# Kernel optimization log

Hardware: AMD Instinct MI355X
Metric: run time of the kernel (lower is better)

## Reference

```python
import jax, jax.numpy as jnp
import numpy as np

N_HEAD = 12
ROPE_BASE = 10000.0


def rotate_half(x):
    h = x.shape[-1] // 2
    x1, x2 = x[..., :h], x[..., h:]
    return jnp.concatenate((-x2, x1), axis=-1)


def rope_cos_sin(T, head_dim, dtype):
    inv_freq = 1.0 / (ROPE_BASE ** (jnp.arange(0, head_dim, 2, dtype=jnp.float32) / head_dim))
    t = jnp.arange(T, dtype=jnp.float32)
    freqs = jnp.einsum('i,j->ij', t, inv_freq)          # [T, head_dim/2]
    emb = jnp.concatenate((freqs, freqs), axis=-1)       # [T, head_dim]
    return jnp.cos(emb).astype(dtype), jnp.sin(emb).astype(dtype)


def setup_inputs() -> dict:
    key = jax.random.key(0)
    ks = jax.random.split(key, 5)
    B, T, C = 1, 4096, 768
    return {
        'x': jax.random.normal(ks[0], (B, T, C), dtype=jnp.float32),
        'w_attn': jax.random.normal(ks[1], (C, 3 * C), dtype=jnp.float32) * (1.0 / np.sqrt(C)),
        'b_attn': jax.random.normal(ks[2], (3 * C,), dtype=jnp.float32) * 0.02,
        'w_proj': jax.random.normal(ks[3], (C, C), dtype=jnp.float32) * (1.0 / np.sqrt(C)),
        'b_proj': jax.random.normal(ks[4], (C,), dtype=jnp.float32) * 0.02,
    }


def reference(x, w_attn, b_attn, w_proj, b_proj):
    B, T, C = x.shape
    H = N_HEAD
    hd = C // H

    qkv = x @ w_attn + b_attn                            # [B, T, 3C]
    q, k, v = jnp.split(qkv, 3, axis=-1)
    q = q.reshape(B, T, H, hd)
    k = k.reshape(B, T, H, hd)
    v = v.reshape(B, T, H, hd)

    cos, sin = rope_cos_sin(T, hd, x.dtype)              # [T, hd]
    cos = cos[None, :, None, :]
    sin = sin[None, :, None, :]
    q = q * cos + rotate_half(q) * sin
    k = k * cos + rotate_half(k) * sin

    # [B, H, T, hd]
    q = q.transpose(0, 2, 1, 3)
    k = k.transpose(0, 2, 1, 3)
    v = v.transpose(0, 2, 1, 3)

    att = jnp.einsum('bhtd,bhsd->bhts', q, k) * (1.0 / np.sqrt(hd))
    causal_mask = jnp.triu(jnp.ones((T, T), dtype=bool), k=1)
    att = jnp.where(causal_mask, -jnp.inf, att)
    att = jax.nn.softmax(att, axis=-1)

    y = jnp.einsum('bhts,bhsd->bhtd', att, v)            # [B, H, T, hd]
    y = y.transpose(0, 2, 1, 3).reshape(B, T, C)
    return y @ w_proj + b_proj
```

## Files before the change

kernel.cpp:

```cpp
#include <hip/hip_runtime.h>
#include <hip/hip_bf16.h>
#include <math.h>

using bf16 = __hip_bfloat16;
typedef __bf16 bf16x8_t __attribute__((ext_vector_type(8)));
typedef float f32x4_t __attribute__((ext_vector_type(4)));

static __device__ __forceinline__ f32x4_t mfma16(bf16x8_t a, bf16x8_t b, f32x4_t c) {
    return __builtin_amdgcn_mfma_f32_16x16x32_bf16(a, b, c, 0, 0, 0);
}

#if __has_builtin(__builtin_amdgcn_exp2f)
#define EXP2F __builtin_amdgcn_exp2f
#else
#define EXP2F exp2f
#endif

static __device__ __forceinline__ void sincos_rev(float rev, float* s, float* c) {
    float f = rev - floorf(rev);
#if __has_builtin(__builtin_amdgcn_sinf) && __has_builtin(__builtin_amdgcn_cosf)
    *s = __builtin_amdgcn_sinf(f);
    *c = __builtin_amdgcn_cosf(f);
#else
    float th = f * 6.2831853071795864f;
    *s = __sinf(th); *c = __cosf(th);
#endif
}

static __device__ __forceinline__ void async16(bf16* lds, const bf16* g) {
#if __has_builtin(__builtin_amdgcn_global_load_lds)
    __builtin_amdgcn_global_load_lds(
        (const __attribute__((address_space(1))) unsigned int*)g,
        (__attribute__((address_space(3))) unsigned int*)lds, 16, 0, 0);
#else
    const int lane = threadIdx.x & 63;
    *reinterpret_cast<float4*>(lds + lane * 8) =
        *reinterpret_cast<const float4*>(g);
#endif
}

static __device__ __forceinline__ float bias_at(const void* b, int i, int isbf) {
    return isbf ? __bfloat162float(((const bf16*)b)[i]) : ((const float*)b)[i];
}

__global__ void detect_kernel(const unsigned short* __restrict__ u16, int* flag) {
    const int lane = threadIdx.x;
    int sane = 0;
#pragma unroll
    for (int j = 0; j < 4; ++j) {
        const unsigned short u = u16[2 * (lane * 4 + j)];
        const int e = (u >> 7) & 0xFF;
        if (u == 0 || (e >= 100 && e <= 150)) sane++;
    }
    for (int off = 32; off; off >>= 1) sane += __shfl_down(sane, off);
    if (lane == 0) *flag = (sane * 2 >= 256) ? 1 : 0;
}

__global__ __launch_bounds__(256) void cast_bf16_kernel(
    const void* __restrict__ in, bf16* __restrict__ out, int n,
    const int* __restrict__ flag) {
    const int i = (blockIdx.x * 256 + threadIdx.x) * 8;
    if (i >= n) return;
    if (*flag) {
        *reinterpret_cast<float4*>(out + i) =
            *reinterpret_cast<const float4*>((const bf16*)in + i);
    } else {
        const float* f = (const float*)in + i;
        const float4 a = *reinterpret_cast<const float4*>(f);
        const float4 b = *reinterpret_cast<const float4*>(f + 4);
        union { float4 v; bf16 e[8]; } u;
        u.e[0] = __float2bfloat16(a.x); u.e[1] = __float2bfloat16(a.y);
        u.e[2] = __float2bfloat16(a.z); u.e[3] = __float2bfloat16(a.w);
        u.e[4] = __float2bfloat16(b.x); u.e[5] = __float2bfloat16(b.y);
        u.e[6] = __float2bfloat16(b.z); u.e[7] = __float2bfloat16(b.w);
        *reinterpret_cast<float4*>(out + i) = u.v;
    }
}

__global__ __launch_bounds__(256) void transpose64_kernel(
    const void* __restrict__ in, bf16* __restrict__ out, int in_ld, int out_ld,
    const int* __restrict__ flag, int force_bf16, int perm) {
    __shared__ bf16 tile[64][72];
    const int isbf = force_bf16 ? 1 : *flag;
    const int c0 = blockIdx.x * 64, r0 = blockIdx.y * 64;
    const int tid = threadIdx.x;
    for (int c = tid; c < 512; c += 256) {
        const int r = c >> 3, co = (c & 7) << 3;
        if (isbf) {
            *reinterpret_cast<float4*>(&tile[r][co]) =
                *reinterpret_cast<const float4*>((const bf16*)in + (size_t)(r0 + r) * in_ld + c0 + co);
        } else {
            const float* f = (const float*)in + (size_t)(r0 + r) * in_ld + c0 + co;
            const float4 a = *reinterpret_cast<const float4*>(f);
            const float4 b = *reinterpret_cast<const float4*>(f + 4);
            tile[r][co + 0] = __float2bfloat16(a.x); tile[r][co + 1] = __float2bfloat16(a.y);
            tile[r][co + 2] = __float2bfloat16(a.z); tile[r][co + 3] = __float2bfloat16(a.w);
            tile[r][co + 4] = __float2bfloat16(b.x); tile[r][co + 5] = __float2bfloat16(b.y);
            tile[r][co + 6] = __float2bfloat16(b.z); tile[r][co + 7] = __float2bfloat16(b.w);
        }
    }
    __syncthreads();
    for (int c = tid; c < 512; c += 256) {
        const int r = c >> 3, co = (c & 7) << 3;
        union { float4 v; bf16 e[8]; } u;
#pragma unroll
        for (int j = 0; j < 8; ++j) {
            const int p = co + j;
            const int src = perm ? (((p & 3) << 4) | (p >> 2)) : p;
            u.e[j] = tile[src][r];
        }
        *reinterpret_cast<float4*>(out + (size_t)(c0 + r) * out_ld + r0 + co) = u.v;
    }
}

__global__ __launch_bounds__(256) void gemm_kernel(
    const bf16* __restrict__ A, const bf16* __restrict__ Bt,
    const void* __restrict__ bias, bf16* __restrict__ C,
    int N, int K, int mode, const int* __restrict__ flag, int flexout) {
    __shared__ bf16 sa[128][40];
    __shared__ bf16 sb[128][40];
    const int isbf = *flag;
    const int f32out = flexout && !isbf;
    const int tid = threadIdx.x, lane = tid & 63, w = tid >> 6;
    const int wm = w >> 1, wn = w & 1, quad = lane >> 4, l16 = lane & 15;
    const int m0 = blockIdx.y * 128, n0 = blockIdx.x * 128;

    f32x4_t acc[4][4];
#pragma unroll
    for (int i = 0; i < 4; ++i)
#pragma unroll
        for (int j = 0; j < 4; ++j) acc[i][j] = (f32x4_t){0.f, 0.f, 0.f, 0.f};

    for (int k0 = 0; k0 < K; k0 += 32) {
        for (int c = tid; c < 512; c += 256) {
            const int r = c >> 2, ko = (c & 3) << 3;
            *reinterpret_cast<float4*>(&sa[r][ko]) =
                *reinterpret_cast<const float4*>(A + (size_t)(m0 + r) * K + k0 + ko);
            *reinterpret_cast<float4*>(&sb[r][ko]) =
                *reinterpret_cast<const float4*>(Bt + (size_t)(n0 + r) * K + k0 + ko);
        }
        __syncthreads();
        bf16x8_t af[4], bg[4];
#pragma unroll
        for (int mi = 0; mi < 4; ++mi)
            af[mi] = *reinterpret_cast<const bf16x8_t*>(&sa[wm * 64 + mi * 16 + l16][quad * 8]);
#pragma unroll
        for (int ni = 0; ni < 4; ++ni)
            bg[ni] = *reinterpret_cast<const bf16x8_t*>(&sb[wn * 64 + ni * 16 + l16][quad * 8]);
#pragma unroll
        for (int mi = 0; mi < 4; ++mi)
#pragma unroll
            for (int ni = 0; ni < 4; ++ni)
                acc[mi][ni] = mfma16(af[mi], bg[ni], acc[mi][ni]);
        __syncthreads();
    }

    const int colbase = n0 + wn * 64;
    const int rowbase = m0 + wm * 64;
    if (mode == 1 && colbase < 1536) {
        const bool isq = colbase < 768;
        const float QS = 0.18033688011112042f;
#pragma unroll
        for (int ni = 0; ni < 2; ++ni) {
            const int d = ni * 16 + l16;
            const int col_lo = colbase + d, col_hi = col_lo + 32;
            const float blo = bias_at(bias, col_lo, isbf);
            const float bhi = bias_at(bias, col_hi, isbf);
            const float invf_rev = powf(10000.0f, -(float)d * (1.0f / 32.0f)) * 0.15915494309189535f;
#pragma unroll
            for (int mi = 0; mi < 4; ++mi) {
#pragma unroll
                for (int rg = 0; rg < 4; ++rg) {
                    const int t = rowbase + mi * 16 + quad * 4 + rg;
                    float sv, cv;
                    sincos_rev((float)t * invf_rev, &sv, &cv);
                    const float lo = acc[mi][ni][rg] + blo;
                    const float hi = acc[mi][ni + 2][rg] + bhi;
                    float nlo = lo * cv - hi * sv;
                    float nhi = hi * cv + lo * sv;
                    if (isq) { nlo *= QS; nhi *= QS; }
                    C[(size_t)t * N + col_lo] = __float2bfloat16(nlo);
                    C[(size_t)t * N + col_hi] = __float2bfloat16(nhi);
                }
            }
        }
    } else {
#pragma unroll
        for (int ni = 0; ni < 4; ++ni) {
            const int col = colbase + ni * 16 + l16;
            const float b = bias_at(bias, col, isbf);
#pragma unroll
            for (int mi = 0; mi < 4; ++mi) {
#pragma unroll
                for (int rg = 0; rg < 4; ++rg) {
                    const int t = rowbase + mi * 16 + quad * 4 + rg;
                    const float v = acc[mi][ni][rg] + b;
                    if (f32out) ((float*)C)[(size_t)t * N + col] = v;
                    else        C[(size_t)t * N + col] = __float2bfloat16(v);
                }
            }
        }
    }
}

__global__ __launch_bounds__(128, 3) void attn_kernel(
    const bf16* __restrict__ qkv, const bf16* __restrict__ Vt,
    bf16* __restrict__ ybuf, bf16* __restrict__ po, float* __restrict__ pl) {
    const int h = blockIdx.y;
    const int bx = blockIdx.x;
    int qt, c, nc;
    if (bx < 16)      { qt = bx;                 c = 0;             nc = 1; }
    else if (bx < 48) { qt = 16 + (bx - 16) / 2; c = (bx - 16) % 2; nc = 2; }
    else if (bx < 96) { qt = 32 + (bx - 48) / 3; c = (bx - 48) % 3; nc = 3; }
    else              { qt = 48 + (bx - 96) / 4; c = (bx - 96) % 4; nc = 4; }
    const int kt0 = c * 16;
    const int kt1 = min(kt0 + 16, qt + 1);

    const int tid = threadIdx.x, lane = tid & 63, w = tid >> 6;
    const int quad = lane >> 4, l16 = lane & 15, sw = l16 & 7;

    __shared__ bf16 Kt[4096];
    __shared__ bf16 Vs[4096];
    __shared__ bf16 Pt[2][2][16][72];

    const int strow = lane >> 3, stslot = lane & 7;
    const bf16* kg[4]; const bf16* vg[4];
#pragma unroll
    for (int i = 0; i < 4; ++i) {
        const int ch = w * 4 + i;
        const int key = ch * 8 + strow;
        kg[i] = qkv + (size_t)key * 2304 + 768 + h * 64 + (stslot ^ (key & 7)) * 8;
        const int d = ch * 8 + strow;
        vg[i] = Vt + (size_t)(h * 64 + d) * 4096 + (stslot ^ (d & 7)) * 8;
    }

    const int qbase = qt * 64 + w * 32;
    bf16x8_t qf[2][2];
#pragma unroll
    for (int f = 0; f < 2; ++f)
#pragma unroll
        for (int kc = 0; kc < 2; ++kc)
            qf[f][kc] = *reinterpret_cast<const bf16x8_t*>(
                qkv + (size_t)(qbase + f * 16 + l16) * 2304 + h * 64 + kc * 32 + quad * 8);

    f32x4_t o[2][4];
#pragma unroll
    for (int f = 0; f < 2; ++f)
#pragma unroll
        for (int dt = 0; dt < 4; ++dt) o[f][dt] = (f32x4_t){0.f, 0.f, 0.f, 0.f};
    float l_i[2][4] = {{0.f, 0.f, 0.f, 0.f}, {0.f, 0.f, 0.f, 0.f}};

    for (int kt = kt0; kt < kt1; ++kt) {
        __syncthreads();
#pragma unroll
        for (int i = 0; i < 4; ++i) {
            async16(&Kt[(w * 4 + i) * 512], kg[i] + (size_t)kt * 64 * 2304);
            async16(&Vs[(w * 4 + i) * 512], vg[i] + (size_t)kt * 64);
        }
        __asm__ __volatile__("s_waitcnt vmcnt(0)" ::: "memory");
        __syncthreads();

        bf16x8_t kf[2][4], vf[2][4];
#pragma unroll
        for (int kc = 0; kc < 2; ++kc)
#pragma unroll
            for (int ct = 0; ct < 4; ++ct)
                kf[kc][ct] = *reinterpret_cast<const bf16x8_t*>(
                    &Kt[((ct * 16 + l16) << 6) + (((kc * 4 + quad) ^ sw) << 3)]);
#pragma unroll
        for (int kc = 0; kc < 2; ++kc)
#pragma unroll
            for (int dt = 0; dt < 4; ++dt)
                vf[kc][dt] = *reinterpret_cast<const bf16x8_t*>(
                    &Vs[((dt * 16 + l16) << 6) + (((kc * 4 + quad) ^ sw) << 3)]);

        f32x4_t s[2][4];
#pragma unroll
        for (int f = 0; f < 2; ++f)
#pragma unroll
            for (int ct = 0; ct < 4; ++ct) {
                s[f][ct] = mfma16(qf[f][0], kf[0][ct], (f32x4_t){0.f, 0.f, 0.f, 0.f});
                s[f][ct] = mfma16(qf[f][1], kf[1][ct], s[f][ct]);
            }

        if (kt == qt) {
#pragma unroll
            for (int f = 0; f < 2; ++f) {
                const int rowb = qbase + f * 16 + quad * 4;
#pragma unroll
                for (int ct = 0; ct < 4; ++ct) {
                    const int key = kt * 64 + ct * 16 + l16;
#pragma unroll
                    for (int rg = 0; rg < 4; ++rg)
                        if (key > rowb + rg) s[f][ct][rg] = -INFINITY;
                }
            }
        }

#pragma unroll
        for (int f = 0; f < 2; ++f)
#pragma unroll
            for (int ct = 0; ct < 4; ++ct)
#pragma unroll
                for (int rg = 0; rg < 4; ++rg) {
                    const float p = EXP2F(s[f][ct][rg]);
                    s[f][ct][rg] = p;
                    l_i[f][rg] += p;
                }

#pragma unroll
        for (int f = 0; f < 2; ++f)
#pragma unroll
            for (int rg = 0; rg < 4; ++rg) {
                union { int2 v; __hip_bfloat162 h2[2]; } pk;
                pk.h2[0] = __float22bfloat162_rn(float2{s[f][0][rg], s[f][1][rg]});
                pk.h2[1] = __float22bfloat162_rn(float2{s[f][2][rg], s[f][3][rg]});
                *reinterpret_cast<int2*>(&Pt[w][f][quad * 4 + rg][l16 * 4]) = pk.v;
            }
        __asm__ __volatile__("s_waitcnt lgkmcnt(0)" ::: "memory");

#pragma unroll
        for (int f = 0; f < 2; ++f)
#pragma unroll
            for (int kc = 0; kc < 2; ++kc) {
                const bf16x8_t pf =
                    *reinterpret_cast<const bf16x8_t*>(&Pt[w][f][l16][kc * 32 + quad * 8]);
#pragma unroll
                for (int dt = 0; dt < 4; ++dt)
                    o[f][dt] = mfma16(pf, vf[kc][dt], o[f][dt]);
            }
    }

#pragma unroll
    for (int off = 1; off <= 8; off <<= 1)
#pragma unroll
        for (int f = 0; f < 2; ++f)
#pragma unroll
            for (int rg = 0; rg < 4; ++rg) l_i[f][rg] += __shfl_xor(l_i[f][rg], off);

    if (nc == 1) {
#pragma unroll
        for (int f = 0; f < 2; ++f) {
            float linv[4];
#pragma unroll
            for (int rg = 0; rg < 4; ++rg)
                linv[rg] = (l_i[f][rg] > 0.f) ? 1.0f / l_i[f][rg] : 0.f;
#pragma unroll
            for (int dt = 0; dt < 4; ++dt)
#pragma unroll
                for (int rg = 0; rg < 4; ++rg)
                    ybuf[(size_t)(qbase + f * 16 + quad * 4 + rg) * 768 + h * 64 + dt * 16 + l16] =
                        __float2bfloat16(o[f][dt][rg] * linv[rg]);
        }
    } else {
#pragma unroll
        for (int f = 0; f < 2; ++f) {
            float linv[4];
#pragma unroll
            for (int rg = 0; rg < 4; ++rg)
                linv[rg] = (l_i[f][rg] > 0.f) ? 1.0f / l_i[f][rg] : 0.f;
#pragma unroll
            for (int dt = 0; dt < 4; ++dt)
#pragma unroll
                for (int rg = 0; rg < 4; ++rg) {
                    const int row = qbase + f * 16 + quad * 4 + rg;
                    po[((size_t)((h << 12) + row) * 4 + c) * 64 + dt * 16 + l16] =
                        __float2bfloat16(o[f][dt][rg] * linv[rg]);
                }
            if (l16 == 0) {
#pragma unroll
                for (int rg = 0; rg < 4; ++rg) {
                    const int row = qbase + f * 16 + quad * 4 + rg;
                    pl[((h << 12) + row) * 4 + c] = l_i[f][rg];
                }
            }
        }
    }
}

__global__ __launch_bounds__(256) void combine_kernel(
    const bf16* __restrict__ po, const float* __restrict__ pl,
    bf16* __restrict__ ybuf) {
    const int g = blockIdx.x * 256 + threadIdx.x;
    if (g >= 12 * 3072 * 64) return;
    const int d = g & 63;
    const int rr = (g >> 6) % 3072;
    const int h = g / (3072 * 64);
    const int r = 1024 + rr;
    const int nc = (r >> 6) / 16 + 1;
    const int base = ((h << 12) + r) * 4;
    float wsum = 0.f, acc = 0.f;
    for (int cc = 0; cc < nc; ++cc) {
        const float wgt = pl[base + cc];
        wsum += wgt;
        acc += wgt * __bfloat162float(po[(size_t)(base + cc) * 64 + d]);
    }
    ybuf[(size_t)r * 768 + h * 64 + d] = __float2bfloat16(acc / wsum);
}

extern "C" void kernel_launch(void* const* d_in, const int* in_sizes, int n_in,
                              void* d_out, int out_size, void* d_ws, size_t ws_size,
                              hipStream_t stream) {
    bf16* qkv  = (bf16*)d_ws;
    bf16* wAT  = qkv + (size_t)4096 * 2304;
    bf16* wPT  = wAT + (size_t)2304 * 768;
    bf16* Vt   = wPT + (size_t)768 * 768;
    bf16* ybuf = Vt + (size_t)768 * 4096;
    bf16* xb   = ybuf + (size_t)4096 * 768;
    int*  flag = (int*)(xb + (size_t)4096 * 768);
    bf16*  po = (bf16*)(flag + 4);
    float* pl = (float*)(po + (size_t)12 * 4096 * 4 * 64);

    detect_kernel<<<1, 64, 0, stream>>>((const unsigned short*)d_in[0], flag);
    cast_bf16_kernel<<<1536, 256, 0, stream>>>(d_in[0], xb, 4096 * 768, flag);
    transpose64_kernel<<<dim3(36, 12), 256, 0, stream>>>(d_in[1], wAT, 2304, 768, flag, 0, 0);
    transpose64_kernel<<<dim3(12, 12), 256, 0, stream>>>(d_in[3], wPT, 768, 768, flag, 0, 0);
    gemm_kernel<<<dim3(18, 32), 256, 0, stream>>>(xb, wAT, d_in[2], qkv, 2304, 768, 1, flag, 0);
    transpose64_kernel<<<dim3(12, 64), 256, 0, stream>>>(qkv + 1536, Vt, 2304, 4096, flag, 1, 1);
    attn_kernel<<<dim3(160, 12), 128, 0, stream>>>(qkv, Vt, ybuf, po, pl);
    combine_kernel<<<9216, 256, 0, stream>>>(po, pl, ybuf);
    gemm_kernel<<<dim3(6, 32), 256, 0, stream>>>(ybuf, wPT, d_in[4], (bf16*)d_out, 768, 768, 0, flag, 1);
}
```

Measured before the change: 216.6 us.

## Fuse prep kernels, use async LDS loads with swizzle in GEMM, retile proj GEMM

Merges dtype detection, the x cast and both weight transposes into a single prep kernel, and recomputes the dtype flag per block so the separate detect launch and flag buffer are no longer needed. The GEMM now loads tiles straight into LDS with global_load_lds over a K-step of 64, using an XOR-swizzled layout to avoid bank conflicts. It is templated on M-tile so the output projection uses 64-row tiles and twice as many blocks. This cuts launch count and global-to-register-to-LDS traffic, but each GEMM iteration still waits on vmcnt(0) with no double buffering, and every block repeats the dtype detection.

```diff
diff --git a/kernel.cpp b/kernel.cpp
--- a/kernel.cpp
+++ b/kernel.cpp
@@ -28,23 +28,13 @@
 }
 
 static __device__ __forceinline__ void async16(bf16* lds, const bf16* g) {
-#if __has_builtin(__builtin_amdgcn_global_load_lds)
     __builtin_amdgcn_global_load_lds(
         (const __attribute__((address_space(1))) unsigned int*)g,
         (__attribute__((address_space(3))) unsigned int*)lds, 16, 0, 0);
-#else
+}
+
+static __device__ __forceinline__ int detect_bf16(const unsigned short* u16) {
     const int lane = threadIdx.x & 63;
-    *reinterpret_cast<float4*>(lds + lane * 8) =
-        *reinterpret_cast<const float4*>(g);
-#endif
-}
-
-static __device__ __forceinline__ float bias_at(const void* b, int i, int isbf) {
-    return isbf ? __bfloat162float(((const bf16*)b)[i]) : ((const float*)b)[i];
-}
-
-__global__ void detect_kernel(const unsigned short* __restrict__ u16, int* flag) {
-    const int lane = threadIdx.x;
     int sane = 0;
 #pragma unroll
     for (int j = 0; j < 4; ++j) {
@@ -52,37 +42,19 @@
         const int e = (u >> 7) & 0xFF;
         if (u == 0 || (e >= 100 && e <= 150)) sane++;
     }
-    for (int off = 32; off; off >>= 1) sane += __shfl_down(sane, off);
-    if (lane == 0) *flag = (sane * 2 >= 256) ? 1 : 0;
-}
-
-__global__ __launch_bounds__(256) void cast_bf16_kernel(
-    const void* __restrict__ in, bf16* __restrict__ out, int n,
-    const int* __restrict__ flag) {
-    const int i = (blockIdx.x * 256 + threadIdx.x) * 8;
-    if (i >= n) return;
-    if (*flag) {
-        *reinterpret_cast<float4*>(out + i) =
-            *reinterpret_cast<const float4*>((const bf16*)in + i);
-    } else {
-        const float* f = (const float*)in + i;
-        const float4 a = *reinterpret_cast<const float4*>(f);
-        const float4 b = *reinterpret_cast<const float4*>(f + 4);
-        union { float4 v; bf16 e[8]; } u;
-        u.e[0] = __float2bfloat16(a.x); u.e[1] = __float2bfloat16(a.y);
-        u.e[2] = __float2bfloat16(a.z); u.e[3] = __float2bfloat16(a.w);
-        u.e[4] = __float2bfloat16(b.x); u.e[5] = __float2bfloat16(b.y);
-        u.e[6] = __float2bfloat16(b.z); u.e[7] = __float2bfloat16(b.w);
-        *reinterpret_cast<float4*>(out + i) = u.v;
-    }
-}
-
-__global__ __launch_bounds__(256) void transpose64_kernel(
-    const void* __restrict__ in, bf16* __restrict__ out, int in_ld, int out_ld,
-    const int* __restrict__ flag, int force_bf16, int perm) {
-    __shared__ bf16 tile[64][72];
-    const int isbf = force_bf16 ? 1 : *flag;
-    const int c0 = blockIdx.x * 64, r0 = blockIdx.y * 64;
+#pragma unroll
+    for (int off = 1; off <= 32; off <<= 1) sane += __shfl_xor(sane, off);
+    return (sane * 2 >= 256) ? 1 : 0;
+}
+
+static __device__ __forceinline__ float bias_at(const void* b, int i, int isbf) {
+    return isbf ? __bfloat162float(((const bf16*)b)[i]) : ((const float*)b)[i];
+}
+
+static __device__ __forceinline__ void transpose_tile(
+    const void* in, bf16* out, int in_ld, int out_ld, int bx, int by,
+    int isbf, int perm, bf16 (*tile)[72]) {
+    const int c0 = bx * 64, r0 = by * 64;
     const int tid = threadIdx.x;
     for (int c = tid; c < 512; c += 256) {
         const int r = c >> 3, co = (c & 7) << 3;
@@ -113,50 +85,110 @@
     }
 }
 
-__global__ __launch_bounds__(256) void gemm_kernel(
+__global__ __launch_bounds__(256) void prep_kernel(
+    const void* __restrict__ x, const void* __restrict__ w_attn,
+    const void* __restrict__ w_proj, bf16* __restrict__ xb,
+    bf16* __restrict__ wAT, bf16* __restrict__ wPT) {
+    __shared__ bf16 tile[64][72];
+    const int isbf = detect_bf16((const unsigned short*)x);
+    const int b = blockIdx.x;
+    if (b < 432) {
+        transpose_tile(w_attn, wAT, 2304, 768, b % 36, b / 36, isbf, 0, tile);
+    } else if (b < 576) {
+        const int bb = b - 432;
+        transpose_tile(w_proj, wPT, 768, 768, bb % 12, bb / 12, isbf, 0, tile);
+    } else {
+        const int i = ((b - 576) * 256 + threadIdx.x) * 8;
+        if (isbf) {
+            *reinterpret_cast<float4*>(xb + i) =
+                *reinterpret_cast<const float4*>((const bf16*)x + i);
+        } else {
+            const float* f = (const float*)x + i;
+            const float4 a = *reinterpret_cast<const float4*>(f);
+            const float4 c = *reinterpret_cast<const float4*>(f + 4);
+            union { float4 v; bf16 e[8]; } u;
+            u.e[0] = __float2bfloat16(a.x); u.e[1] = __float2bfloat16(a.y);
+            u.e[2] = __float2bfloat16(a.z); u.e[3] = __float2bfloat16(a.w);
+            u.e[4] = __float2bfloat16(c.x); u.e[5] = __float2bfloat16(c.y);
+            u.e[6] = __float2bfloat16(c.z); u.e[7] = __float2bfloat16(c.w);
+            *reinterpret_cast<float4*>(xb + i) = u.v;
+        }
+    }
+}
+
+__global__ __launch_bounds__(256) void vt_kernel(
+    const bf16* __restrict__ v, bf16* __restrict__ Vt) {
+    __shared__ bf16 tile[64][72];
+    transpose_tile(v, Vt, 2304, 4096, blockIdx.x, blockIdx.y, 1, 1, tile);
+}
+
+template <int MI>
+__global__ __launch_bounds__(256, MI == 4 ? 3 : 4) void gemm_kernel(
     const bf16* __restrict__ A, const bf16* __restrict__ Bt,
     const void* __restrict__ bias, bf16* __restrict__ C,
-    int N, int K, int mode, const int* __restrict__ flag, int flexout) {
-    __shared__ bf16 sa[128][40];
-    __shared__ bf16 sb[128][40];
-    const int isbf = *flag;
-    const int f32out = flexout && !isbf;
+    const unsigned short* __restrict__ xdet, int N, int K, int mode, int flexout) {
+    constexpr int MT = MI * 32;
+    __shared__ bf16 sa[MT * 64];
+    __shared__ bf16 sb[128 * 64];
     const int tid = threadIdx.x, lane = tid & 63, w = tid >> 6;
     const int wm = w >> 1, wn = w & 1, quad = lane >> 4, l16 = lane & 15;
-    const int m0 = blockIdx.y * 128, n0 = blockIdx.x * 128;
-
-    f32x4_t acc[4][4];
-#pragma unroll
-    for (int i = 0; i < 4; ++i)
+    const int m0 = blockIdx.y * MT, n0 = blockIdx.x * 128;
+    const int strow = lane >> 3, stslot = lane & 7;
+
+    const bf16* ag[MI]; const bf16* bgp[4];
+#pragma unroll
+    for (int i = 0; i < MI; ++i) {
+        const int r = (w * MI + i) * 8 + strow;
+        ag[i] = A + (size_t)(m0 + r) * K + (stslot ^ (r & 7)) * 8;
+    }
+#pragma unroll
+    for (int i = 0; i < 4; ++i) {
+        const int r = (w * 4 + i) * 8 + strow;
+        bgp[i] = Bt + (size_t)(n0 + r) * K + (stslot ^ (r & 7)) * 8;
+    }
+
+    f32x4_t acc[MI][4];
+#pragma unroll
+    for (int i = 0; i < MI; ++i)
 #pragma unroll
         for (int j = 0; j < 4; ++j) acc[i][j] = (f32x4_t){0.f, 0.f, 0.f, 0.f};
 
-    for (int k0 = 0; k0 < K; k0 += 32) {
-        for (int c = tid; c < 512; c += 256) {
-            const int r = c >> 2, ko = (c & 3) << 3;
-            *reinterpret_cast<float4*>(&sa[r][ko]) =
-                *reinterpret_cast<const float4*>(A + (size_t)(m0 + r) * K + k0 + ko);
-            *reinterpret_cast<float4*>(&sb[r][ko]) =
-                *reinterpret_cast<const float4*>(Bt + (size_t)(n0 + r) * K + k0 + ko);
-        }
+    for (int k0 = 0; k0 < K; k0 += 64) {
         __syncthreads();
-        bf16x8_t af[4], bg[4];
-#pragma unroll
-        for (int mi = 0; mi < 4; ++mi)
-            af[mi] = *reinterpret_cast<const bf16x8_t*>(&sa[wm * 64 + mi * 16 + l16][quad * 8]);
-#pragma unroll
-        for (int ni = 0; ni < 4; ++ni)
-            bg[ni] = *reinterpret_cast<const bf16x8_t*>(&sb[wn * 64 + ni * 16 + l16][quad * 8]);
-#pragma unroll
-        for (int mi = 0; mi < 4; ++mi)
-#pragma unroll
-            for (int ni = 0; ni < 4; ++ni)
-                acc[mi][ni] = mfma16(af[mi], bg[ni], acc[mi][ni]);
+#pragma unroll
+        for (int i = 0; i < MI; ++i) async16(&sa[(w * MI + i) * 512], ag[i] + k0);
+#pragma unroll
+        for (int i = 0; i < 4; ++i)  async16(&sb[(w * 4 + i) * 512], bgp[i] + k0);
+        __asm__ __volatile__("s_waitcnt vmcnt(0)" ::: "memory");
         __syncthreads();
-    }
-
+
+#pragma unroll
+        for (int kk = 0; kk < 2; ++kk) {
+            bf16x8_t af[MI], bf_[4];
+#pragma unroll
+            for (int mi = 0; mi < MI; ++mi) {
+                const int r = wm * (MI * 16) + mi * 16 + l16;
+                af[mi] = *reinterpret_cast<const bf16x8_t*>(
+                    &sa[r * 64 + (((kk * 4 + quad) ^ (r & 7)) << 3)]);
+            }
+#pragma unroll
+            for (int ni = 0; ni < 4; ++ni) {
+                const int r = wn * 64 + ni * 16 + l16;
+                bf_[ni] = *reinterpret_cast<const bf16x8_t*>(
+                    &sb[r * 64 + (((kk * 4 + quad) ^ (r & 7)) << 3)]);
+            }
+#pragma unroll
+            for (int mi = 0; mi < MI; ++mi)
+#pragma unroll
+                for (int ni = 0; ni < 4; ++ni)
+                    acc[mi][ni] = mfma16(af[mi], bf_[ni], acc[mi][ni]);
+        }
+    }
+
+    const int isbf = detect_bf16(xdet);
+    const int f32out = flexout && !isbf;
     const int colbase = n0 + wn * 64;
-    const int rowbase = m0 + wm * 64;
+    const int rowbase = m0 + wm * (MI * 16);
     if (mode == 1 && colbase < 1536) {
         const bool isq = colbase < 768;
         const float QS = 0.18033688011112042f;
@@ -168,7 +200,7 @@
             const float bhi = bias_at(bias, col_hi, isbf);
             const float invf_rev = powf(10000.0f, -(float)d * (1.0f / 32.0f)) * 0.15915494309189535f;
 #pragma unroll
-            for (int mi = 0; mi < 4; ++mi) {
+            for (int mi = 0; mi < MI; ++mi) {
 #pragma unroll
                 for (int rg = 0; rg < 4; ++rg) {
                     const int t = rowbase + mi * 16 + quad * 4 + rg;
@@ -190,7 +222,7 @@
             const int col = colbase + ni * 16 + l16;
             const float b = bias_at(bias, col, isbf);
 #pragma unroll
-            for (int mi = 0; mi < 4; ++mi) {
+            for (int mi = 0; mi < MI; ++mi) {
 #pragma unroll
                 for (int rg = 0; rg < 4; ++rg) {
                     const int t = rowbase + mi * 16 + quad * 4 + rg;
@@ -407,17 +439,16 @@
     bf16* Vt   = wPT + (size_t)768 * 768;
     bf16* ybuf = Vt + (size_t)768 * 4096;
     bf16* xb   = ybuf + (size_t)4096 * 768;
-    int*  flag = (int*)(xb + (size_t)4096 * 768);
-    bf16*  po = (bf16*)(flag + 4);
-    float* pl = (float*)(po + (size_t)12 * 4096 * 4 * 64);
-
-    detect_kernel<<<1, 64, 0, stream>>>((const unsigned short*)d_in[0], flag);
-    cast_bf16_kernel<<<1536, 256, 0, stream>>>(d_in[0], xb, 4096 * 768, flag);
-    transpose64_kernel<<<dim3(36, 12), 256, 0, stream>>>(d_in[1], wAT, 2304, 768, flag, 0, 0);
-    transpose64_kernel<<<dim3(12, 12), 256, 0, stream>>>(d_in[3], wPT, 768, 768, flag, 0, 0);
-    gemm_kernel<<<dim3(18, 32), 256, 0, stream>>>(xb, wAT, d_in[2], qkv, 2304, 768, 1, flag, 0);
-    transpose64_kernel<<<dim3(12, 64), 256, 0, stream>>>(qkv + 1536, Vt, 2304, 4096, flag, 1, 1);
+    bf16* po   = xb + (size_t)4096 * 768;
+    float* pl  = (float*)(po + (size_t)12 * 4096 * 4 * 64);
+    const unsigned short* xdet = (const unsigned short*)d_in[0];
+
+    prep_kernel<<<2112, 256, 0, stream>>>(d_in[0], d_in[1], d_in[3], xb, wAT, wPT);
+    gemm_kernel<4><<<dim3(18, 32), 256, 0, stream>>>(
+        xb, wAT, d_in[2], qkv, xdet, 2304, 768, 1, 0);
+    vt_kernel<<<dim3(12, 64), 256, 0, stream>>>(qkv + 1536, Vt);
     attn_kernel<<<dim3(160, 12), 128, 0, stream>>>(qkv, Vt, ybuf, po, pl);
     combine_kernel<<<9216, 256, 0, stream>>>(po, pl, ybuf);
-    gemm_kernel<<<dim3(6, 32), 256, 0, stream>>>(ybuf, wPT, d_in[4], (bf16*)d_out, 768, 768, 0, flag, 1);
-}
+    gemm_kernel<2><<<dim3(6, 64), 256, 0, stream>>>(
+        ybuf, wPT, d_in[4], (bf16*)d_out, xdet, 768, 768, 0, 1);
+}
```

After: 189.2 us. 1.14x faster.
